# Kernel tuning notes

Hardware: AMD Instinct MI355X
Metric: run time of the kernel (lower is better)

The kernel has to match this reference:

```python
import jax, jax.numpy as jnp
import numpy as np

IN_F, OUT_F = 4096, 16384


def setup_inputs() -> dict:
    key = jax.random.key(0)
    k1, k2, k3, k4 = jax.random.split(key, 4)
    x = jax.random.normal(k1, (8, 64, IN_F), dtype=jnp.float32)
    # int8-valued quantized weight stored as int32 (values in [-127, 127])
    Wq = jax.random.randint(k2, (OUT_F, IN_F), -127, 128, dtype=jnp.int32)
    # per-output-row scales (absmax/60 style): small positive floats
    row_scales = jax.random.uniform(k3, (OUT_F,), dtype=jnp.float32, minval=1e-4, maxval=0.05)
    bias = jax.random.normal(k4, (OUT_F,), dtype=jnp.float32)
    return {"x": x, "Wq": Wq, "row_scales": row_scales, "bias": bias}


def reference(x, Wq, row_scales, bias):
    # Row-wise dequantization: W[o, i] = Wq[o, i] * row_scales[o]
    W = Wq.astype(x.dtype) * row_scales[:, None].astype(x.dtype)  # [out, in]
    # Wq is [out, in]; x last dim == in, so the transpose branch runs:
    # Y = x @ W.T + bias
    Y = jnp.einsum('bsi,oi->bso', x, W) + bias.astype(x.dtype)
    return Y
```

## Files before the change

### kernel.cpp

```cpp
#include <hip/hip_runtime.h>

#define IN_F 4096
#define OUT_F 16384
#define M_ROWS 512

#define BM 256
#define BN 128
#define BK 64
#define NKT (IN_F / BK)
#define THREADS 512

typedef __bf16 bf16x8_t __attribute__((ext_vector_type(8)));
typedef float f32x4_t __attribute__((ext_vector_type(4)));
typedef int i32x4_t __attribute__((ext_vector_type(4)));

__device__ __forceinline__ void gld16(const void* g, void* l) {
    __builtin_amdgcn_global_load_lds(
        (const __attribute__((address_space(1))) void*)g,
        (__attribute__((address_space(3))) void*)l,
        16 , 0, 0);
}

__global__ __launch_bounds__(256)
void xpack_kernel(const float* __restrict__ x, __bf16* __restrict__ xp) {
    const int tid = blockIdx.x * 256 + (int)threadIdx.x;
    const int e0 = tid * 8;
    const int tile = e0 >> 14;
    const int within = e0 & 16383;
    const int row = within >> 6;
    const int rem0 = within & 63;
    const int mt = tile >> 6;
    const int kt = tile & 63;
    const int grow = mt * 256 + row;
    const int gcol = kt * 64 + (rem0 ^ ((row & 7) << 3));
    const float* src = x + (size_t)grow * IN_F + gcol;
    f32x4_t a = *(const f32x4_t*)(src);
    f32x4_t b = *(const f32x4_t*)(src + 4);
    bf16x8_t o;
    o[0] = (__bf16)a[0]; o[1] = (__bf16)a[1]; o[2] = (__bf16)a[2]; o[3] = (__bf16)a[3];
    o[4] = (__bf16)b[0]; o[5] = (__bf16)b[1]; o[6] = (__bf16)b[2]; o[7] = (__bf16)b[3];
    *(bf16x8_t*)(xp + e0) = o;
}

__global__ __launch_bounds__(THREADS, 2)
void qgemm3_kernel(const __bf16* __restrict__ xp, const int* __restrict__ Wq,
                   const float* __restrict__ scales, const float* __restrict__ bias,
                   float* __restrict__ out) {
    __shared__ __align__(16) unsigned char sA[2][BM * BK * 2];
    __shared__ __align__(16) unsigned char sB[2][BN * BK * 2];

    const int bid = (int)blockIdx.x;
    const int g = (bid & 7) * 32 + (bid >> 3);
    const int mt = g & 1;
    const int nt = g >> 1;
    const int brow = mt * BM;
    const int bcol = nt * BN;

    const int t = (int)threadIdx.x;
    const int lane = t & 63;
    const int wid = t >> 6;
    const int wr = wid >> 1;
    const int wc = wid & 1;

    const int rB = t >> 3;
    const int cB = (t & 7) * 8;
    const int* wg = Wq + (size_t)(bcol + rB) * IN_F + cB;
    const int offB = rB * 128 + ((cB * 2) ^ ((rB & 7) << 4));

    const __bf16* xt = xp + (size_t)(mt * NKT) * (BM * BK) + t * 8;
    const int ldsAoff = wid * 1024;

    f32x4_t acc[4][4];
#pragma unroll
    for (int i = 0; i < 4; ++i)
#pragma unroll
        for (int j = 0; j < 4; ++j) {
            f32x4_t z = {0.f, 0.f, 0.f, 0.f};
            acc[i][j] = z;
        }

    const int arow = wr * 64 + (lane & 15);
    const int browf = wc * 64 + (lane & 15);
    const int kb = (lane >> 4) * 16;

    i32x4_t bvA[4], bvB[4];
    bf16x8_t af[2][4], bf[2][4];

#define ISSUE_A(KT1, PB)                                              \
    do {                                                              \
        const __bf16* s_ = xt + (size_t)(KT1) * (BM * BK);            \
        unsigned char* d_ = &sA[PB][0] + ldsAoff;                     \
        gld16(s_, d_);                                                \
        gld16(s_ + 4096, d_ + 8192);                                  \
        gld16(s_ + 8192, d_ + 16384);                                 \
        gld16(s_ + 12288, d_ + 24576);                                \
    } while (0)

#define ISSUE_B(KT2, BV)                                              \
    do {                                                              \
        const int* p_ = wg + (size_t)(KT2) * BK;                      \
        BV[0] = *(const i32x4_t*)(p_);                                \
        BV[1] = *(const i32x4_t*)(p_ + 4);                            \
        BV[2] = *(const i32x4_t*)(p_ + (size_t)64 * IN_F);            \
        BV[3] = *(const i32x4_t*)(p_ + (size_t)64 * IN_F + 4);        \
    } while (0)

#define WRITE_B(BV, PB)                                               \
    do {                                                              \
        bf16x8_t w0_, w1_;                                            \
        _Pragma("unroll") for (int j_ = 0; j_ < 4; ++j_) {            \
            w0_[j_] = (__bf16)(float)BV[0][j_];                       \
            w0_[4 + j_] = (__bf16)(float)BV[1][j_];                   \
            w1_[j_] = (__bf16)(float)BV[2][j_];                       \
            w1_[4 + j_] = (__bf16)(float)BV[3][j_];                   \
        }                                                             \
        *(bf16x8_t*)(&sB[PB][0] + offB) = w0_;                        \
        *(bf16x8_t*)(&sB[PB][0] + offB + 8192) = w1_;                 \
    } while (0)

#define READ_FRAGS(CUR)                                                              \
    do {                                                                             \
        _Pragma("unroll") for (int m_ = 0; m_ < 4; ++m_) {                           \
            const int r_ = arow + m_ * 16;                                           \
            const int x_ = (r_ & 7) << 4;                                            \
            af[0][m_] = *(const bf16x8_t*)(&sA[CUR][0] + r_ * 128 + ((kb) ^ x_));    \
            af[1][m_] = *(const bf16x8_t*)(&sA[CUR][0] + r_ * 128 + ((64 + kb) ^ x_)); \
        }                                                                            \
        _Pragma("unroll") for (int n_ = 0; n_ < 4; ++n_) {                           \
            const int r_ = browf + n_ * 16;                                          \
            const int x_ = (r_ & 7) << 4;                                            \
            bf[0][n_] = *(const bf16x8_t*)(&sB[CUR][0] + r_ * 128 + ((kb) ^ x_));    \
            bf[1][n_] = *(const bf16x8_t*)(&sB[CUR][0] + r_ * 128 + ((64 + kb) ^ x_)); \
        }                                                                            \
    } while (0)

#define MFMA_KS(KS)                                                       \
    do {                                                                  \
        _Pragma("unroll") for (int m_ = 0; m_ < 4; ++m_)                  \
            _Pragma("unroll") for (int n_ = 0; n_ < 4; ++n_)              \
                acc[m_][n_] = __builtin_amdgcn_mfma_f32_16x16x32_bf16(    \
                    af[KS][m_], bf[KS][n_], acc[m_][n_], 0, 0, 0);        \
    } while (0)

#define KT_STEP(CUR, KT, BVW, BVI)                                        \
    do {                                                                  \
        asm volatile("s_waitcnt vmcnt(4) lgkmcnt(0)" ::: "memory");       \
        __builtin_amdgcn_s_barrier();                                     \
        __builtin_amdgcn_sched_barrier(0);                                \
        READ_FRAGS(CUR);                                                  \
        {                                                                 \
            const int k1_ = ((KT) + 1 < NKT) ? (KT) + 1 : NKT - 1;        \
            ISSUE_A(k1_, (CUR) ^ 1);                                      \
        }                                                                 \
        __builtin_amdgcn_sched_barrier(0);                                \
        __builtin_amdgcn_s_setprio(1);                                    \
        MFMA_KS(0);                                                       \
        __builtin_amdgcn_s_setprio(0);                                    \
        WRITE_B(BVW, (CUR) ^ 1);                                          \
        {                                                                 \
            const int k2_ = ((KT) + 2 < NKT) ? (KT) + 2 : NKT - 1;        \
            ISSUE_B(k2_, BVI);                                            \
        }                                                                 \
        __builtin_amdgcn_s_setprio(1);                                    \
        MFMA_KS(1);                                                       \
        __builtin_amdgcn_s_setprio(0);                                    \
    } while (0)

    ISSUE_A(0, 0);
    ISSUE_B(0, bvA);
    asm volatile("s_waitcnt vmcnt(0)" ::: "memory");
    WRITE_B(bvA, 0);
    ISSUE_B(1, bvB);

#pragma unroll 1
    for (int kt = 0; kt < NKT; kt += 2) {
        KT_STEP(0, kt, bvB, bvA);
        KT_STEP(1, kt + 1, bvA, bvB);
    }

    const int orow = brow + wr * 64 + ((lane >> 4) << 2);
    const int ocol = bcol + wc * 64 + (lane & 15);
#pragma unroll
    for (int n = 0; n < 4; ++n) {
        const int c = ocol + n * 16;
        const float sc = scales[c];
        const float bs = bias[c];
#pragma unroll
        for (int m = 0; m < 4; ++m) {
            const int r = orow + m * 16;
            float* po = out + (size_t)r * OUT_F + c;
#pragma unroll
            for (int j = 0; j < 4; ++j) {
                po[(size_t)j * OUT_F] = acc[m][n][j] * sc + bs;
            }
        }
    }
#undef ISSUE_A
#undef ISSUE_B
#undef WRITE_B
#undef READ_FRAGS
#undef MFMA_KS
#undef KT_STEP
}

__global__ __launch_bounds__(256, 2)
void qgemm_fallback(const float* __restrict__ x, const int* __restrict__ Wq,
                    const float* __restrict__ scales, const float* __restrict__ bias,
                    float* __restrict__ out) {
    __shared__ __align__(16) unsigned char fA[128 * 64 * 2];
    __shared__ __align__(16) unsigned char fB[128 * 64 * 2];

    const int bid = (int)blockIdx.x;
    const int g = (bid & 7) * 64 + (bid >> 3);
    const int mt = g & 3;
    const int nt = g >> 2;
    const int brow = mt * 128;
    const int bcol = nt * 128;

    const int t = (int)threadIdx.x;
    const int lane = t & 63;
    const int wid = t >> 6;
    const int wr = wid >> 1;
    const int wc = wid & 1;

    const int srow = t >> 4;
    const int sc4 = t & 15;

    const float* xg = x + (size_t)(brow + srow) * IN_F + sc4 * 4;
    const int* wg = Wq + (size_t)(bcol + srow) * IN_F + sc4 * 4;

    f32x4_t acc[4][4];
#pragma unroll
    for (int i = 0; i < 4; ++i)
#pragma unroll
        for (int j = 0; j < 4; ++j) {
            f32x4_t z = {0.f, 0.f, 0.f, 0.f};
            acc[i][j] = z;
        }

    const int frow_a = wr * 64 + (lane & 15);
    const int frow_b = wc * 64 + (lane & 15);
    const int fk = (lane >> 4) * 16;

#pragma unroll 1
    for (int kt = 0; kt < IN_F / 64; ++kt) {
        const int k0 = kt * 64;
        f32x4_t av[8];
        i32x4_t bv[8];
#pragma unroll
        for (int i = 0; i < 8; ++i) {
            av[i] = *(const f32x4_t*)(xg + k0 + (size_t)i * 16 * IN_F);
            bv[i] = *(const i32x4_t*)(wg + k0 + (size_t)i * 16 * IN_F);
        }
        __syncthreads();
#pragma unroll
        for (int i = 0; i < 8; ++i) {
            const int row = srow + i * 16;
            unsigned off = (unsigned)(row * 128 + sc4 * 8);
            off ^= (unsigned)(row & 7) << 4;
            __bf16 pa[4], pb[4];
#pragma unroll
            for (int j = 0; j < 4; ++j) {
                pa[j] = (__bf16)av[i][j];
                pb[j] = (__bf16)(float)bv[i][j];
            }
            *(unsigned long long*)(fA + off) = *(unsigned long long*)pa;
            *(unsigned long long*)(fB + off) = *(unsigned long long*)pb;
        }
        __syncthreads();
#pragma unroll
        for (int ks = 0; ks < 2; ++ks) {
            bf16x8_t afv[4], bfv[4];
#pragma unroll
            for (int m = 0; m < 4; ++m) {
                const int row = frow_a + m * 16;
                afv[m] = *(const bf16x8_t*)(fA + (row * 128 + ((ks * 64 + fk) ^ ((row & 7) << 4))));
            }
#pragma unroll
            for (int n = 0; n < 4; ++n) {
                const int row = frow_b + n * 16;
                bfv[n] = *(const bf16x8_t*)(fB + (row * 128 + ((ks * 64 + fk) ^ ((row & 7) << 4))));
            }
#pragma unroll
            for (int m = 0; m < 4; ++m)
#pragma unroll
                for (int n = 0; n < 4; ++n)
                    acc[m][n] = __builtin_amdgcn_mfma_f32_16x16x32_bf16(
                        afv[m], bfv[n], acc[m][n], 0, 0, 0);
        }
    }

    const int orow = brow + wr * 64 + ((lane >> 4) << 2);
    const int ocol = bcol + wc * 64 + (lane & 15);
#pragma unroll
    for (int n = 0; n < 4; ++n) {
        const int c = ocol + n * 16;
        const float sc = scales[c];
        const float bs = bias[c];
#pragma unroll
        for (int m = 0; m < 4; ++m) {
            const int r = orow + m * 16;
            float* po = out + (size_t)r * OUT_F + c;
#pragma unroll
            for (int j = 0; j < 4; ++j) {
                po[(size_t)j * OUT_F] = acc[m][n][j] * sc + bs;
            }
        }
    }
}

extern "C" void kernel_launch(void* const* d_in, const int* in_sizes, int n_in,
                              void* d_out, int out_size, void* d_ws, size_t ws_size,
                              hipStream_t stream) {
    const float* x = (const float*)d_in[0];
    const int* Wq = (const int*)d_in[1];
    const float* scales = (const float*)d_in[2];
    const float* bias = (const float*)d_in[3];
    float* out = (float*)d_out;

    const size_t xp_bytes = (size_t)M_ROWS * IN_F * 2;
    const bool pre = (ws_size >= xp_bytes) && (d_ws != nullptr);

    if (pre) {
        __bf16* xp = (__bf16*)d_ws;
        xpack_kernel<<<dim3((M_ROWS * IN_F / 8) / 256), dim3(256), 0, stream>>>(x, xp);
        qgemm3_kernel<<<dim3(256), dim3(THREADS), 0, stream>>>(xp, Wq, scales, bias, out);
    } else {
        qgemm_fallback<<<dim3(512), dim3(256), 0, stream>>>(x, Wq, scales, bias, out);
    }
}
```

Measured before the change: 116.4 us.

## Use full-M 512x64 tiles so each weight row is read exactly once

The GEMM block tile becomes 512 rows by 64 columns, so each block covers all M rows and each int32 weight element is loaded and converted to bf16 once, not once per M tile. The grid grows to 256 blocks along N only, and the x packing layout changes to match the single M tile. The A tile in LDS doubles, raising LDS use per block to about 144 KB, which likely limits occupancy to one block per CU, and A traffic from L2 rises since every block streams all of x.

```diff
diff --git a/kernel.cpp b/kernel.cpp
--- a/kernel.cpp
+++ b/kernel.cpp
@@ -4,11 +4,12 @@
 #define OUT_F 16384
 #define M_ROWS 512
 
-#define BM 256
-#define BN 128
+#define BM 512
+#define BN 64
 #define BK 64
 #define NKT (IN_F / BK)
 #define THREADS 512
+#define A_TILE_ELEMS (BM * BK)
 
 typedef __bf16 bf16x8_t __attribute__((ext_vector_type(8)));
 typedef float f32x4_t __attribute__((ext_vector_type(4)));
@@ -25,15 +26,12 @@
 void xpack_kernel(const float* __restrict__ x, __bf16* __restrict__ xp) {
     const int tid = blockIdx.x * 256 + (int)threadIdx.x;
     const int e0 = tid * 8;
-    const int tile = e0 >> 14;
-    const int within = e0 & 16383;
+    const int tile = e0 >> 15;
+    const int within = e0 & 32767;
     const int row = within >> 6;
     const int rem0 = within & 63;
-    const int mt = tile >> 6;
-    const int kt = tile & 63;
-    const int grow = mt * 256 + row;
-    const int gcol = kt * 64 + (rem0 ^ ((row & 7) << 3));
-    const float* src = x + (size_t)grow * IN_F + gcol;
+    const int gcol = tile * 64 + (rem0 ^ ((row & 7) << 3));
+    const float* src = x + (size_t)row * IN_F + gcol;
     f32x4_t a = *(const f32x4_t*)(src);
     f32x4_t b = *(const f32x4_t*)(src + 4);
     bf16x8_t o;
@@ -43,31 +41,23 @@
 }
 
 __global__ __launch_bounds__(THREADS, 2)
-void qgemm3_kernel(const __bf16* __restrict__ xp, const int* __restrict__ Wq,
+void qgemm4_kernel(const __bf16* __restrict__ xp, const int* __restrict__ Wq,
                    const float* __restrict__ scales, const float* __restrict__ bias,
                    float* __restrict__ out) {
     __shared__ __align__(16) unsigned char sA[2][BM * BK * 2];
     __shared__ __align__(16) unsigned char sB[2][BN * BK * 2];
 
-    const int bid = (int)blockIdx.x;
-    const int g = (bid & 7) * 32 + (bid >> 3);
-    const int mt = g & 1;
-    const int nt = g >> 1;
-    const int brow = mt * BM;
-    const int bcol = nt * BN;
-
+    const int bcol = (int)blockIdx.x * BN;
     const int t = (int)threadIdx.x;
     const int lane = t & 63;
     const int wid = t >> 6;
-    const int wr = wid >> 1;
-    const int wc = wid & 1;
 
     const int rB = t >> 3;
-    const int cB = (t & 7) * 8;
-    const int* wg = Wq + (size_t)(bcol + rB) * IN_F + cB;
-    const int offB = rB * 128 + ((cB * 2) ^ ((rB & 7) << 4));
-
-    const __bf16* xt = xp + (size_t)(mt * NKT) * (BM * BK) + t * 8;
+    const int c8 = (t & 7) * 8;
+    const int* wg = Wq + (size_t)(bcol + rB) * IN_F + c8;
+    const int offB = rB * 128 + ((c8 * 2) ^ ((rB & 7) << 4));
+
+    const __bf16* xt = xp + t * 8;
     const int ldsAoff = wid * 1024;
 
     f32x4_t acc[4][4];
@@ -79,43 +69,36 @@
             acc[i][j] = z;
         }
 
-    const int arow = wr * 64 + (lane & 15);
-    const int browf = wc * 64 + (lane & 15);
+    const int arow = wid * 64 + (lane & 15);
+    const int browf = lane & 15;
     const int kb = (lane >> 4) * 16;
 
-    i32x4_t bvA[4], bvB[4];
+    i32x4_t bvA[2], bvB[2];
     bf16x8_t af[2][4], bf[2][4];
 
-#define ISSUE_A(KT1, PB)                                              \
-    do {                                                              \
-        const __bf16* s_ = xt + (size_t)(KT1) * (BM * BK);            \
-        unsigned char* d_ = &sA[PB][0] + ldsAoff;                     \
-        gld16(s_, d_);                                                \
-        gld16(s_ + 4096, d_ + 8192);                                  \
-        gld16(s_ + 8192, d_ + 16384);                                 \
-        gld16(s_ + 12288, d_ + 24576);                                \
-    } while (0)
-
-#define ISSUE_B(KT2, BV)                                              \
-    do {                                                              \
-        const int* p_ = wg + (size_t)(KT2) * BK;                      \
-        BV[0] = *(const i32x4_t*)(p_);                                \
-        BV[1] = *(const i32x4_t*)(p_ + 4);                            \
-        BV[2] = *(const i32x4_t*)(p_ + (size_t)64 * IN_F);            \
-        BV[3] = *(const i32x4_t*)(p_ + (size_t)64 * IN_F + 4);        \
-    } while (0)
-
-#define WRITE_B(BV, PB)                                               \
-    do {                                                              \
-        bf16x8_t w0_, w1_;                                            \
-        _Pragma("unroll") for (int j_ = 0; j_ < 4; ++j_) {            \
-            w0_[j_] = (__bf16)(float)BV[0][j_];                       \
-            w0_[4 + j_] = (__bf16)(float)BV[1][j_];                   \
-            w1_[j_] = (__bf16)(float)BV[2][j_];                       \
-            w1_[4 + j_] = (__bf16)(float)BV[3][j_];                   \
-        }                                                             \
-        *(bf16x8_t*)(&sB[PB][0] + offB) = w0_;                        \
-        *(bf16x8_t*)(&sB[PB][0] + offB + 8192) = w1_;                 \
+#define ISSUE_A(KT1, PB)                                            \
+    do {                                                            \
+        const __bf16* s_ = xt + (size_t)(KT1) * A_TILE_ELEMS;       \
+        unsigned char* d_ = &sA[PB][0] + ldsAoff;                   \
+        _Pragma("unroll") for (int i_ = 0; i_ < 8; ++i_)            \
+            gld16(s_ + i_ * 4096, d_ + i_ * 8192);                  \
+    } while (0)
+
+#define ISSUE_B(KT2, BV)                                            \
+    do {                                                            \
+        const int* p_ = wg + (size_t)(KT2) * BK;                    \
+        BV[0] = *(const i32x4_t*)(p_);                              \
+        BV[1] = *(const i32x4_t*)(p_ + 4);                          \
+    } while (0)
+
+#define WRITE_B(BV, PB)                                             \
+    do {                                                            \
+        bf16x8_t w_;                                                \
+        _Pragma("unroll") for (int j_ = 0; j_ < 4; ++j_) {          \
+            w_[j_] = (__bf16)(float)BV[0][j_];                      \
+            w_[4 + j_] = (__bf16)(float)BV[1][j_];                  \
+        }                                                           \
+        *(bf16x8_t*)(&sB[PB][0] + offB) = w_;                       \
     } while (0)
 
 #define READ_FRAGS(CUR)                                                              \
@@ -144,7 +127,8 @@
 
 #define KT_STEP(CUR, KT, BVW, BVI)                                        \
     do {                                                                  \
-        asm volatile("s_waitcnt vmcnt(4) lgkmcnt(0)" ::: "memory");       \
+        asm volatile("s_waitcnt vmcnt(2) lgkmcnt(0)" ::: "memory");       \
+        __builtin_amdgcn_sched_barrier(0);                                \
         __builtin_amdgcn_s_barrier();                                     \
         __builtin_amdgcn_sched_barrier(0);                                \
         READ_FRAGS(CUR);                                                  \
@@ -178,16 +162,16 @@
         KT_STEP(1, kt + 1, bvA, bvB);
     }
 
-    const int orow = brow + wr * 64 + ((lane >> 4) << 2);
-    const int ocol = bcol + wc * 64 + (lane & 15);
+    const int orow0 = wid * 64 + ((lane >> 4) << 2);
+    const int ocol0 = bcol + (lane & 15);
 #pragma unroll
     for (int n = 0; n < 4; ++n) {
-        const int c = ocol + n * 16;
+        const int c = ocol0 + n * 16;
         const float sc = scales[c];
         const float bs = bias[c];
 #pragma unroll
         for (int m = 0; m < 4; ++m) {
-            const int r = orow + m * 16;
+            const int r = orow0 + m * 16;
             float* po = out + (size_t)r * OUT_F + c;
 #pragma unroll
             for (int j = 0; j < 4; ++j) {
@@ -324,7 +308,7 @@
     if (pre) {
         __bf16* xp = (__bf16*)d_ws;
         xpack_kernel<<<dim3((M_ROWS * IN_F / 8) / 256), dim3(256), 0, stream>>>(x, xp);
-        qgemm3_kernel<<<dim3(256), dim3(THREADS), 0, stream>>>(xp, Wq, scales, bias, out);
+        qgemm4_kernel<<<dim3(OUT_F / BN), dim3(THREADS), 0, stream>>>(xp, Wq, scales, bias, out);
     } else {
         qgemm_fallback<<<dim3(512), dim3(256), 0, stream>>>(x, Wq, scales, bias, out);
     }
```

New measurement: 119.3 us. +2.5%, slower.
